# Kernel optimization log

Measured on AMD Instinct MI355X. Metric: run time of the kernel, lower is better.

## Reference

```python
import jax, jax.numpy as jnp
import numpy as np
import math

N_NODES = 50000
N_EDGES = 800000
IN_FEATS = 128
HID = 64
OUT = 2
D = 2  # num_layers


def calc_thetas(d):
    """Beta-distribution polynomial coefficients (ascending order), matching
    sympy.poly((x/2)**i * (1-x/2)**(d-i) / Beta(i+1, d+1-i)) with inverted coeffs."""
    thetas = []
    for i in range(d + 1):
        p1 = np.zeros(i + 1)
        p1[-1] = 0.5 ** i  # (x/2)^i, ascending coeffs
        p2 = np.array([math.comb(d - i, j) * (-0.5) ** j for j in range(d - i + 1)])  # (1-x/2)^(d-i)
        beta = math.factorial(i) * math.factorial(d - i) / math.factorial(d + 1)
        thetas.append((np.convolve(p1, p2) / beta).tolist())
    return thetas


def poly_branch(h, src, dst, thetas):
    """Run all PolyConv filters on activated features h; concat along feature dim."""
    n = h.shape[0]
    deg = jnp.zeros((n,), h.dtype).at[dst].add(jnp.ones((dst.shape[0],), h.dtype))
    dinv = jnp.clip(deg, 1.0, None) ** -0.5  # D^{-1/2} of in-degrees, clamped min 1
    dinv = dinv[:, None]
    outs = []
    for th in thetas:
        f = h
        acc = th[0] * h
        for k in range(1, len(th)):
            # feat <- feat - D^{-1/2} A D^{-1/2} feat  (copy_u / sum aggregation)
            agg = jax.ops.segment_sum((f * dinv)[src], dst, num_segments=n)
            f = f - agg * dinv
            acc = acc + th[k] * f
        outs.append(acc)
    return jnp.concatenate(outs, axis=-1)


def setup_inputs() -> dict:
    key = jax.random.key(0)
    ks = jax.random.split(key, 12)
    inp = {
        "x": jax.random.normal(ks[0], (N_NODES, IN_FEATS), jnp.float32),
        "sim_x": jax.random.normal(ks[1], (N_NODES, IN_FEATS), jnp.float32),
        "src": jax.random.randint(ks[2], (N_EDGES,), 0, N_NODES, jnp.int32),
        "dst": jax.random.randint(ks[3], (N_EDGES,), 0, N_NODES, jnp.int32),
        "sim_src": jax.random.randint(ks[4], (N_EDGES,), 0, N_NODES, jnp.int32),
        "sim_dst": jax.random.randint(ks[5], (N_EDGES,), 0, N_NODES, jnp.int32),
        "W1_o": jax.random.normal(ks[6], (IN_FEATS, HID), jnp.float32) / np.sqrt(IN_FEATS),
        "b1_o": jnp.zeros((HID,), jnp.float32),
        "W1_s": jax.random.normal(ks[7], (IN_FEATS, HID), jnp.float32) / np.sqrt(IN_FEATS),
        "b1_s": jnp.zeros((HID,), jnp.float32),
        "Wm1": jax.random.normal(ks[8], (HID * (D + 1) * 2, HID), jnp.float32) / np.sqrt(HID * (D + 1) * 2),
        "bm1": jnp.zeros((HID,), jnp.float32),
        "Wm2": jax.random.normal(ks[9], (HID, OUT), jnp.float32) / np.sqrt(HID),
        "bm2": jnp.zeros((OUT,), jnp.float32),
    }
    return inp


def reference(x, sim_x, src, dst, sim_src, sim_dst,
              W1_o, b1_o, W1_s, b1_s, Wm1, bm1, Wm2, bm2):
    thetas_o = calc_thetas(D)
    thetas_s = [[4.0] * (D + 1) for _ in range(D + 1)]  # conv_s uses constant theta=4

    h = jax.nn.relu(x @ W1_o + b1_o)
    h_final = poly_branch(h, src, dst, thetas_o)      # [N, HID*(D+1)]

    sh = jax.nn.relu(sim_x @ W1_s + b1_s)
    sim_h_final = poly_branch(sh, sim_src, sim_dst, thetas_s)

    h_all = jnp.concatenate([h_final, sim_h_final], axis=-1)  # [N, HID*(D+1)*2]
    logits = jax.nn.relu(h_all @ Wm1 + bm1) @ Wm2 + bm2
    return (h_all, logits)
```

## Files before the change

### kernel.cpp

```cpp
#include <hip/hip_runtime.h>
#include <hip/hip_fp16.h>


#define KB_BITS 10
#define KMAX 64
#define PCHUNK 4096
#define PVPT 16

__global__ __launch_bounds__(256) void bhist_kernel(
    const int* __restrict__ dst, const int* __restrict__ sim_dst,
    int* __restrict__ bhist, int E, int Es) {
    __shared__ int h[2 * KMAX];
    int tid = threadIdx.x;
    if (tid < 2 * KMAX) h[tid] = 0;
    __syncthreads();
    int total = E + Es;
    for (int e = blockIdx.x * 256 + tid; e < total; e += gridDim.x * 256) {
        if (e < E) atomicAdd(&h[dst[e] >> KB_BITS], 1);
        else       atomicAdd(&h[KMAX + (sim_dst[e - E] >> KB_BITS)], 1);
    }
    __syncthreads();
    if (tid < 2 * KMAX && h[tid]) atomicAdd(&bhist[tid], h[tid]);
}

__global__ __launch_bounds__(128) void bscan_kernel(
    const int* __restrict__ bhist, int* __restrict__ brow,
    int* __restrict__ gcur) {
    int g = threadIdx.x >> 6, lane = threadIdx.x & 63;
    int v = bhist[g * KMAX + lane];
    int inc = v;
    #pragma unroll
    for (int off = 1; off < 64; off <<= 1) {
        int u = __shfl_up(inc, off);
        if (lane >= off) inc += u;
    }
    int ex = inc - v;
    brow[g * (KMAX + 1) + lane] = ex;
    if (lane == 63) brow[g * (KMAX + 1) + KMAX] = inc;
    gcur[g * KMAX + lane] = ex;
}

__global__ __launch_bounds__(256) void partition_kernel(
    const int* __restrict__ src, const int* __restrict__ dst,
    const int* __restrict__ sim_src, const int* __restrict__ sim_dst,
    int* __restrict__ gcur, unsigned* __restrict__ staged,
    int E, int Es, int nbo) {
    int b = blockIdx.x;
    const int* S; const int* D; int Eg; int goff; unsigned* stg;
    if (b < nbo) { S = src; D = dst; Eg = E; goff = 0; stg = staged; }
    else { b -= nbo; S = sim_src; D = sim_dst; Eg = Es; goff = KMAX; stg = staged + E; }
    int e0 = b * PCHUNK;
    int cnt_blk = Eg - e0; if (cnt_blk > PCHUNK) cnt_blk = PCHUNK;
    __shared__ int hist[KMAX], basep[KMAX], cur[KMAX], gbase[KMAX];
    __shared__ unsigned srt[PCHUNK];
    int tid = threadIdx.x;
    if (tid < KMAX) hist[tid] = 0;
    __syncthreads();
    unsigned full[PVPT];
    #pragma unroll
    for (int i = 0; i < PVPT; ++i) {
        int idx = i * 256 + tid;
        if (idx < cnt_blk) {
            int e = e0 + idx;
            int d = D[e];
            unsigned bk = (unsigned)d >> KB_BITS;
            full[i] = (bk << 26) | ((unsigned)S[e] << KB_BITS) |
                      (unsigned)(d & ((1 << KB_BITS) - 1));
            atomicAdd(&hist[bk], 1);
        } else full[i] = 0xFFFFFFFFu;
    }
    __syncthreads();
    if (tid < 64) {
        int v = hist[tid];
        int inc = v;
        #pragma unroll
        for (int off = 1; off < 64; off <<= 1) {
            int u = __shfl_up(inc, off);
            if (tid >= off) inc += u;
        }
        int ex = inc - v;
        basep[tid] = ex;
        cur[tid] = ex;
        gbase[tid] = v ? atomicAdd(&gcur[goff + tid], v) : 0;
    }
    __syncthreads();
    #pragma unroll
    for (int i = 0; i < PVPT; ++i) {
        unsigned f = full[i];
        if (f != 0xFFFFFFFFu) {
            unsigned bk = f >> 26;
            int slot = atomicAdd(&cur[bk], 1);
            srt[slot] = f;
        }
    }
    __syncthreads();
    for (int slot = tid; slot < cnt_blk; slot += 256) {
        unsigned f = srt[slot];
        unsigned bk = f >> 26;
        int gpos = gbase[bk] + (slot - basep[bk]);
        stg[gpos] = f & 0x3FFFFFFu;
    }
}

__global__ __launch_bounds__(512) void place_kernel(
    const unsigned* __restrict__ staged, const int* __restrict__ brow,
    int* __restrict__ row_o, int* __restrict__ row_s,
    int* __restrict__ esrc_o, int* __restrict__ esrc_s,
    float* __restrict__ dinv, int N, int K, int E) {
    int b = blockIdx.x;
    const unsigned* stg; const int* br; int* row; int* esrc; float* dv;
    if (b < K) { stg = staged; br = brow; row = row_o; esrc = esrc_o; dv = dinv; }
    else { b -= K; stg = staged + E; br = brow + (KMAX + 1); row = row_s; esrc = esrc_s; dv = dinv + N; }
    int node0 = b << KB_BITS;
    int nn = N - node0; if (nn > (1 << KB_BITS)) nn = (1 << KB_BITS);
    int seg0 = br[b], seg1 = br[b + 1];
    __shared__ int ncnt[1 << KB_BITS];
    __shared__ int wsum[8];
    int tid = threadIdx.x;
    for (int i = tid; i < (1 << KB_BITS); i += 512) ncnt[i] = 0;
    __syncthreads();
    for (int j = seg0 + tid; j < seg1; j += 512)
        atomicAdd(&ncnt[stg[j] & ((1 << KB_BITS) - 1)], 1);
    __syncthreads();
    int i0 = tid * 2;
    int v0 = ncnt[i0], v1 = ncnt[i0 + 1];
    int s = v0 + v1;
    int inc = s;
    #pragma unroll
    for (int off = 1; off < 64; off <<= 1) {
        int u = __shfl_up(inc, off);
        if ((tid & 63) >= off) inc += u;
    }
    if ((tid & 63) == 63) wsum[tid >> 6] = inc;
    __syncthreads();
    int wo = 0;
    for (int w = 0; w < (tid >> 6); ++w) wo += wsum[w];
    int ex = seg0 + wo + inc - s;
    if (i0 < nn) {
        row[node0 + i0] = ex;
        dv[node0 + i0] = rsqrtf((float)(v0 > 1 ? v0 : 1));
    }
    if (i0 + 1 < nn) {
        row[node0 + i0 + 1] = ex + v0;
        dv[node0 + i0 + 1] = rsqrtf((float)(v1 > 1 ? v1 : 1));
    }
    if (b == K - 1 && tid == 0) row[N] = br[K];
    __syncthreads();
    ncnt[i0] = ex;
    ncnt[i0 + 1] = ex + v0;
    __syncthreads();
    for (int j = seg0 + tid; j < seg1; j += 512) {
        unsigned f = stg[j];
        int pos = atomicAdd(&ncnt[f & ((1 << KB_BITS) - 1)], 1);
        esrc[pos] = (int)(f >> KB_BITS);
    }
}

__global__ __launch_bounds__(256) void in_gemm_kernel(
    const float* __restrict__ x, const float* __restrict__ W,
    const float* __restrict__ b, float* __restrict__ out, int off,
    __half* __restrict__ h16, const float* __restrict__ dinvv, int n) {
    __shared__ float xs[64][132];
    __shared__ float Wf[128][68];
    int tid = threadIdx.x;
    int node0 = blockIdx.x * 64;
    const float4* wsrc = (const float4*)W;
    for (int i = tid; i < 2048; i += 256)
        *(float4*)&Wf[i >> 4][(i & 15) * 4] = wsrc[i];
    const float4* xsrc = (const float4*)x;
    for (int i = tid; i < 2048; i += 256) {
        int nl = i >> 5, c = i & 31;
        int node = node0 + nl;
        float4 v = make_float4(0.f, 0.f, 0.f, 0.f);
        if (node < n) v = xsrc[(long)node * 32 + c];
        *(float4*)&xs[nl][c * 4] = v;
    }
    __syncthreads();
    int tx = tid & 15, ty = tid >> 4;
    float acc[4][4] = {};
    #pragma unroll 2
    for (int k = 0; k < 128; k += 4) {
        float4 a[4], bb[4];
        #pragma unroll
        for (int i = 0; i < 4; ++i) a[i] = *(const float4*)&xs[ty * 4 + i][k];
        #pragma unroll
        for (int j = 0; j < 4; ++j) bb[j] = *(const float4*)&Wf[k + j][tx * 4];
        #pragma unroll
        for (int i = 0; i < 4; ++i) {
            acc[i][0] = fmaf(a[i].x, bb[0].x, acc[i][0]);
            acc[i][1] = fmaf(a[i].x, bb[0].y, acc[i][1]);
            acc[i][2] = fmaf(a[i].x, bb[0].z, acc[i][2]);
            acc[i][3] = fmaf(a[i].x, bb[0].w, acc[i][3]);
            acc[i][0] = fmaf(a[i].y, bb[1].x, acc[i][0]);
            acc[i][1] = fmaf(a[i].y, bb[1].y, acc[i][1]);
            acc[i][2] = fmaf(a[i].y, bb[1].z, acc[i][2]);
            acc[i][3] = fmaf(a[i].y, bb[1].w, acc[i][3]);
            acc[i][0] = fmaf(a[i].z, bb[2].x, acc[i][0]);
            acc[i][1] = fmaf(a[i].z, bb[2].y, acc[i][1]);
            acc[i][2] = fmaf(a[i].z, bb[2].z, acc[i][2]);
            acc[i][3] = fmaf(a[i].z, bb[2].w, acc[i][3]);
            acc[i][0] = fmaf(a[i].w, bb[3].x, acc[i][0]);
            acc[i][1] = fmaf(a[i].w, bb[3].y, acc[i][1]);
            acc[i][2] = fmaf(a[i].w, bb[3].z, acc[i][2]);
            acc[i][3] = fmaf(a[i].w, bb[3].w, acc[i][3]);
        }
    }
    float4 bias = *(const float4*)&b[tx * 4];
    #pragma unroll
    for (int i = 0; i < 4; ++i) {
        int node = node0 + ty * 4 + i;
        if (node >= n) break;
        float4 r;
        r.x = fmaxf(acc[i][0] + bias.x, 0.0f);
        r.y = fmaxf(acc[i][1] + bias.y, 0.0f);
        r.z = fmaxf(acc[i][2] + bias.z, 0.0f);
        r.w = fmaxf(acc[i][3] + bias.w, 0.0f);
        *(float4*)&out[(long)node * 384 + off + tx * 4] = r;
        if (h16) {
            float dvn = dinvv[node];
            __half hh[4];
            hh[0] = __float2half_rn(r.x * dvn);
            hh[1] = __float2half_rn(r.y * dvn);
            hh[2] = __float2half_rn(r.z * dvn);
            hh[3] = __float2half_rn(r.w * dvn);
            *(float2*)&h16[(long)node * 64 + tx * 4] = *(float2*)hh;
        }
    }
}

__global__ __launch_bounds__(256) void hop1_kernel(
    const int* __restrict__ row_o, const int* __restrict__ esrc_o, const float* __restrict__ dinv_o,
    const int* __restrict__ row_s, const int* __restrict__ esrc_s, const float* __restrict__ dinv_s,
    const __half* __restrict__ h16_o, const __half* __restrict__ h16_s,
    __half* __restrict__ g16_o, __half* __restrict__ g16_s,
    float* __restrict__ hall, int n, int nb) {
    int b = blockIdx.x;
    const int* row; const int* esrc; const float* dinv; const __half* h16; __half* g16; int base;
    if (b < nb) { row = row_o; esrc = esrc_o; dinv = dinv_o; h16 = h16_o; g16 = g16_o; base = 0; }
    else { b -= nb; row = row_s; esrc = esrc_s; dinv = dinv_s; h16 = h16_s; g16 = g16_s; base = 192; }
    int d = b * 4 + (threadIdx.x >> 6);
    if (d >= n) return;
    int lane = threadIdx.x & 63;
    int p = row[d], end = row[d + 1];
    long ob = (long)d * 384 + lane;
    float dd = dinv[d];
    float f0 = hall[ob + base];
    float a0 = 0.f, a1 = 0.f, a2 = 0.f, a3 = 0.f;
    for (; p + 8 <= end; p += 8) {
        int s0 = esrc[p], s1 = esrc[p + 1], s2 = esrc[p + 2], s3 = esrc[p + 3];
        int s4 = esrc[p + 4], s5 = esrc[p + 5], s6 = esrc[p + 6], s7 = esrc[p + 7];
        a0 += __half2float(h16[(long)s0 * 64 + lane]);
        a1 += __half2float(h16[(long)s1 * 64 + lane]);
        a2 += __half2float(h16[(long)s2 * 64 + lane]);
        a3 += __half2float(h16[(long)s3 * 64 + lane]);
        a0 += __half2float(h16[(long)s4 * 64 + lane]);
        a1 += __half2float(h16[(long)s5 * 64 + lane]);
        a2 += __half2float(h16[(long)s6 * 64 + lane]);
        a3 += __half2float(h16[(long)s7 * 64 + lane]);
    }
    for (; p < end; ++p) {
        int s = esrc[p];
        a0 += __half2float(h16[(long)s * 64 + lane]);
    }
    float acc = (a0 + a1) + (a2 + a3);
    float f1 = f0 - acc * dd;
    hall[ob + base + 64] = f1;
    g16[(long)d * 64 + lane] = __float2half_rn(f1 * dd);
}

__global__ __launch_bounds__(256) void hop2_kernel(
    const int* __restrict__ row_o, const int* __restrict__ esrc_o, const float* __restrict__ dinv_o,
    const int* __restrict__ row_s, const int* __restrict__ esrc_s, const float* __restrict__ dinv_s,
    const __half* __restrict__ g16_o, const __half* __restrict__ g16_s,
    float* __restrict__ hall, int n, int nb) {
    int b = blockIdx.x;
    bool ortho = b < nb;
    const int* row; const int* esrc; const float* dinv; const __half* g16; int base;
    if (ortho) { row = row_o; esrc = esrc_o; dinv = dinv_o; g16 = g16_o; base = 0; }
    else { b -= nb; row = row_s; esrc = esrc_s; dinv = dinv_s; g16 = g16_s; base = 192; }
    int d = b * 4 + (threadIdx.x >> 6);
    if (d >= n) return;
    int lane = threadIdx.x & 63;
    int p = row[d], end = row[d + 1];
    long ob = (long)d * 384 + lane;
    float dd = dinv[d];
    float f0 = hall[ob + base];
    float f1 = hall[ob + base + 64];
    float a0 = 0.f, a1 = 0.f, a2 = 0.f, a3 = 0.f;
    for (; p + 8 <= end; p += 8) {
        int s0 = esrc[p], s1 = esrc[p + 1], s2 = esrc[p + 2], s3 = esrc[p + 3];
        int s4 = esrc[p + 4], s5 = esrc[p + 5], s6 = esrc[p + 6], s7 = esrc[p + 7];
        a0 += __half2float(g16[(long)s0 * 64 + lane]);
        a1 += __half2float(g16[(long)s1 * 64 + lane]);
        a2 += __half2float(g16[(long)s2 * 64 + lane]);
        a3 += __half2float(g16[(long)s3 * 64 + lane]);
        a0 += __half2float(g16[(long)s4 * 64 + lane]);
        a1 += __half2float(g16[(long)s5 * 64 + lane]);
        a2 += __half2float(g16[(long)s6 * 64 + lane]);
        a3 += __half2float(g16[(long)s7 * 64 + lane]);
    }
    for (; p < end; ++p) {
        int s = esrc[p];
        a0 += __half2float(g16[(long)s * 64 + lane]);
    }
    float acc = (a0 + a1) + (a2 + a3);
    float f2 = f1 - acc * dd;
    if (ortho) {
        hall[ob]       = 3.0f * f0 - 3.0f * f1 + 0.75f * f2;
        hall[ob + 64]  = 3.0f * f1 - 1.5f * f2;
        hall[ob + 128] = 0.75f * f2;
    } else {
        float ss = 4.0f * (f0 + f1 + f2);
        hall[ob + 192] = ss; hall[ob + 256] = ss; hall[ob + 320] = ss;
    }
}

__global__ __launch_bounds__(256) void gather2_kernel(
    const int* __restrict__ row_o, const int* __restrict__ esrc_o, const float* __restrict__ dinv_o,
    const int* __restrict__ row_s, const int* __restrict__ esrc_s, const float* __restrict__ dinv_s,
    float* __restrict__ hall, int in_off_o, int in_off_s, int n, int nb) {
    int b = blockIdx.x;
    const int* row; const int* esrc; const float* dinv; int in_off;
    if (b < nb) { row = row_o; esrc = esrc_o; dinv = dinv_o; in_off = in_off_o; }
    else { b -= nb; row = row_s; esrc = esrc_s; dinv = dinv_s; in_off = in_off_s; }
    int d = b * 4 + (threadIdx.x >> 6);
    if (d >= n) return;
    int lane = threadIdx.x & 63;
    int p = row[d], end = row[d + 1];
    const float* fin = hall + in_off;
    float a0 = 0.f, a1 = 0.f, a2 = 0.f, a3 = 0.f;
    for (; p + 4 <= end; p += 4) {
        int s0 = esrc[p], s1 = esrc[p + 1], s2 = esrc[p + 2], s3 = esrc[p + 3];
        a0 = fmaf(fin[(long)s0 * 384 + lane], dinv[s0], a0);
        a1 = fmaf(fin[(long)s1 * 384 + lane], dinv[s1], a1);
        a2 = fmaf(fin[(long)s2 * 384 + lane], dinv[s2], a2);
        a3 = fmaf(fin[(long)s3 * 384 + lane], dinv[s3], a3);
    }
    for (; p < end; ++p) {
        int s = esrc[p];
        a0 = fmaf(fin[(long)s * 384 + lane], dinv[s], a0);
    }
    float acc = (a0 + a1) + (a2 + a3);
    long ob = (long)d * 384 + lane;
    hall[ob + in_off + 64] = fin[ob] - acc * dinv[d];
}

__global__ __launch_bounds__(256) void combine_kernel(float* __restrict__ h, int nf) {
    int i = blockIdx.x * 256 + threadIdx.x;
    if (i >= nf) return;
    long ob = (long)(i >> 6) * 384 + (i & 63);
    float f0v = h[ob], f1v = h[ob + 64], f2v = h[ob + 128];
    h[ob]       = 3.0f * f0v - 3.0f * f1v + 0.75f * f2v;
    h[ob + 64]  = 3.0f * f1v - 1.5f * f2v;
    h[ob + 128] = 0.75f * f2v;
    float ss = 4.0f * (h[ob + 192] + h[ob + 256] + h[ob + 320]);
    h[ob + 192] = ss; h[ob + 256] = ss; h[ob + 320] = ss;
}

__global__ __launch_bounds__(256) void mlp_kernel(
    const float* __restrict__ hall, const float* __restrict__ Wm1,
    const float* __restrict__ bm1, const float* __restrict__ Wm2,
    const float* __restrict__ bm2, float* __restrict__ logits, int n) {
    __shared__ float xs[64][132];
    __shared__ float Wf[128][68];
    int tid = threadIdx.x;
    int node0 = blockIdx.x * 64;
    int tx = tid & 15, ty = tid >> 4;
    float acc[4][4] = {};
    const float4* wsrc = (const float4*)Wm1;
    const float4* hsrc = (const float4*)hall;
    for (int c = 0; c < 3; ++c) {
        __syncthreads();
        for (int i = tid; i < 2048; i += 256)
            *(float4*)&Wf[i >> 4][(i & 15) * 4] = wsrc[c * 2048 + i];
        for (int i = tid; i < 2048; i += 256) {
            int nl = i >> 5, cc = i & 31;
            int node = node0 + nl;
            float4 v = make_float4(0.f, 0.f, 0.f, 0.f);
            if (node < n) v = hsrc[(long)node * 96 + c * 32 + cc];
            *(float4*)&xs[nl][cc * 4] = v;
        }
        __syncthreads();
        #pragma unroll 2
        for (int k = 0; k < 128; k += 4) {
            float4 a[4], bb[4];
            #pragma unroll
            for (int i = 0; i < 4; ++i) a[i] = *(const float4*)&xs[ty * 4 + i][k];
            #pragma unroll
            for (int j = 0; j < 4; ++j) bb[j] = *(const float4*)&Wf[k + j][tx * 4];
            #pragma unroll
            for (int i = 0; i < 4; ++i) {
                acc[i][0] = fmaf(a[i].x, bb[0].x, acc[i][0]);
                acc[i][1] = fmaf(a[i].x, bb[0].y, acc[i][1]);
                acc[i][2] = fmaf(a[i].x, bb[0].z, acc[i][2]);
                acc[i][3] = fmaf(a[i].x, bb[0].w, acc[i][3]);
                acc[i][0] = fmaf(a[i].y, bb[1].x, acc[i][0]);
                acc[i][1] = fmaf(a[i].y, bb[1].y, acc[i][1]);
                acc[i][2] = fmaf(a[i].y, bb[1].z, acc[i][2]);
                acc[i][3] = fmaf(a[i].y, bb[1].w, acc[i][3]);
                acc[i][0] = fmaf(a[i].z, bb[2].x, acc[i][0]);
                acc[i][1] = fmaf(a[i].z, bb[2].y, acc[i][1]);
                acc[i][2] = fmaf(a[i].z, bb[2].z, acc[i][2]);
                acc[i][3] = fmaf(a[i].z, bb[2].w, acc[i][3]);
                acc[i][0] = fmaf(a[i].w, bb[3].x, acc[i][0]);
                acc[i][1] = fmaf(a[i].w, bb[3].y, acc[i][1]);
                acc[i][2] = fmaf(a[i].w, bb[3].z, acc[i][2]);
                acc[i][3] = fmaf(a[i].w, bb[3].w, acc[i][3]);
            }
        }
    }
    __syncthreads();
    float4 bias = *(const float4*)&bm1[tx * 4];
    #pragma unroll
    for (int i = 0; i < 4; ++i) {
        xs[ty * 4 + i][tx * 4 + 0] = fmaxf(acc[i][0] + bias.x, 0.0f);
        xs[ty * 4 + i][tx * 4 + 1] = fmaxf(acc[i][1] + bias.y, 0.0f);
        xs[ty * 4 + i][tx * 4 + 2] = fmaxf(acc[i][2] + bias.z, 0.0f);
        xs[ty * 4 + i][tx * 4 + 3] = fmaxf(acc[i][3] + bias.w, 0.0f);
    }
    __syncthreads();
    if (tid < 128) {
        int nl = tid >> 1, o = tid & 1;
        int node = node0 + nl;
        if (node < n) {
            float p = bm2[o];
            #pragma unroll 8
            for (int k = 0; k < 64; ++k) p = fmaf(xs[nl][k], Wm2[k * 2 + o], p);
            logits[(long)node * 2 + o] = p;
        }
    }
}

extern "C" void kernel_launch(void* const* d_in, const int* in_sizes, int n_in,
                              void* d_out, int out_size, void* d_ws, size_t ws_size,
                              hipStream_t stream) {
    const float* x     = (const float*)d_in[0];
    const float* sim_x = (const float*)d_in[1];
    const int* src     = (const int*)d_in[2];
    const int* dst     = (const int*)d_in[3];
    const int* sim_src = (const int*)d_in[4];
    const int* sim_dst = (const int*)d_in[5];
    const float* W1_o = (const float*)d_in[6];
    const float* b1_o = (const float*)d_in[7];
    const float* W1_s = (const float*)d_in[8];
    const float* b1_s = (const float*)d_in[9];
    const float* Wm1  = (const float*)d_in[10];
    const float* bm1  = (const float*)d_in[11];
    const float* Wm2  = (const float*)d_in[12];
    const float* bm2  = (const float*)d_in[13];

    const int N  = in_sizes[0] / 128;
    const int E  = in_sizes[2];
    const int Es = in_sizes[4];
    const int NF = N * 64;
    const int K  = (N + (1 << KB_BITS) - 1) >> KB_BITS;

    float* hall = (float*)d_out;
    float* lgt  = hall + (long)N * 384;
    float* dinv = lgt;
    float* dinv_o = dinv;
    float* dinv_s = dinv + N;

    int* row_o  = (int*)d_ws;
    int* row_s  = row_o + (N + 1);
    int* esrc_o = row_s + (N + 1);
    int* esrc_s = esrc_o + E;
    int* bhist  = esrc_s + Es;
    int* brow   = bhist + 2 * KMAX;
    int* gcur   = brow + 2 * (KMAX + 1);
    __half* h16_o = (__half*)(gcur + 2 * KMAX);
    __half* h16_s = h16_o + (long)N * 64;
    __half* g16_o = h16_s + (long)N * 64;
    __half* g16_s = g16_o + (long)N * 64;
    size_t need_f16 = (size_t)((char*)(g16_s + (long)N * 64) - (char*)d_ws);
    bool f16path = ws_size >= need_f16;
    unsigned* staged = (unsigned*)h16_o;

    int nb4  = (N + 3) / 4;
    int nb64 = (N + 63) / 64;
    int nfb  = (NF + 255) / 256;
    int nbo  = (E + PCHUNK - 1) / PCHUNK;
    int nbs  = (Es + PCHUNK - 1) / PCHUNK;

    hipMemsetAsync(bhist, 0, (size_t)(2 * KMAX) * sizeof(int), stream);
    bhist_kernel<<<256, 256, 0, stream>>>(dst, sim_dst, bhist, E, Es);
    bscan_kernel<<<1, 128, 0, stream>>>(bhist, brow, gcur);
    partition_kernel<<<nbo + nbs, 256, 0, stream>>>(src, dst, sim_src, sim_dst,
                                                    gcur, staged, E, Es, nbo);
    place_kernel<<<2 * K, 512, 0, stream>>>(staged, brow, row_o, row_s,
                                            esrc_o, esrc_s, dinv, N, K, E);

    in_gemm_kernel<<<nb64, 256, 0, stream>>>(x, W1_o, b1_o, hall, 0,
                                             f16path ? h16_o : (__half*)nullptr, dinv_o, N);
    in_gemm_kernel<<<nb64, 256, 0, stream>>>(sim_x, W1_s, b1_s, hall, 192,
                                             f16path ? h16_s : (__half*)nullptr, dinv_s, N);

    if (f16path) {
        hop1_kernel<<<2 * nb4, 256, 0, stream>>>(row_o, esrc_o, dinv_o,
                                                 row_s, esrc_s, dinv_s,
                                                 h16_o, h16_s, g16_o, g16_s,
                                                 hall, N, nb4);
        hop2_kernel<<<2 * nb4, 256, 0, stream>>>(row_o, esrc_o, dinv_o,
                                                 row_s, esrc_s, dinv_s,
                                                 g16_o, g16_s, hall, N, nb4);
    } else {
        gather2_kernel<<<2 * nb4, 256, 0, stream>>>(row_o, esrc_o, dinv_o,
                                                    row_s, esrc_s, dinv_s,
                                                    hall, 0, 192, N, nb4);
        gather2_kernel<<<2 * nb4, 256, 0, stream>>>(row_o, esrc_o, dinv_o,
                                                    row_s, esrc_s, dinv_s,
                                                    hall, 64, 256, N, nb4);
        combine_kernel<<<nfb, 256, 0, stream>>>(hall, NF);
    }

    mlp_kernel<<<nb64, 256, 0, stream>>>(hall, Wm1, bm1, Wm2, bm2, lgt, N);
}
```

Baseline: 432.3 us.

## Drop fp32 intermediate traffic, recompute features from fp16, fold MLP weights

The input GEMM no longer writes fp32 features to the output on the fp16 path. The hop kernels rebuild f0 and f1 from the scaled fp16 buffers with sqrt(deg) and compute dinv from the CSR row extents. Block indices are interleaved so both graph branches run side by side. Since the sim branch writes three identical 4*(f0+f1+f2) columns, its three Wm1 slices are pre-summed so the MLP reads two K-chunks instead of three. This cuts global memory traffic and MLP FLOPs. The cost is that f0 and f1 now carry fp16 rounding, which may hurt accuracy.

```diff
diff --git a/kernel.cpp b/kernel.cpp
--- a/kernel.cpp
+++ b/kernel.cpp
@@ -154,6 +154,16 @@
         int pos = atomicAdd(&ncnt[f & ((1 << KB_BITS) - 1)], 1);
         esrc[pos] = (int)(f >> KB_BITS);
     }
+}
+
+__global__ __launch_bounds__(256) void fold_kernel(
+    const float* __restrict__ Wm1, float* __restrict__ w1f) {
+    int i = blockIdx.x * 256 + threadIdx.x;
+    if (i >= 256 * 64) return;
+    int k = i >> 6, j = i & 63;
+    float v = Wm1[k * 64 + j];
+    if (k >= 192) v += Wm1[(k + 64) * 64 + j] + Wm1[(k + 128) * 64 + j];
+    w1f[i] = v;
 }
 
 __global__ __launch_bounds__(256) void in_gemm_kernel(
@@ -215,7 +225,7 @@
         r.y = fmaxf(acc[i][1] + bias.y, 0.0f);
         r.z = fmaxf(acc[i][2] + bias.z, 0.0f);
         r.w = fmaxf(acc[i][3] + bias.w, 0.0f);
-        *(float4*)&out[(long)node * 384 + off + tx * 4] = r;
+        if (out) *(float4*)&out[(long)node * 384 + off + tx * 4] = r;
         if (h16) {
             float dvn = dinvv[node];
             __half hh[4];
@@ -229,22 +239,26 @@
 }
 
 __global__ __launch_bounds__(256) void hop1_kernel(
-    const int* __restrict__ row_o, const int* __restrict__ esrc_o, const float* __restrict__ dinv_o,
-    const int* __restrict__ row_s, const int* __restrict__ esrc_s, const float* __restrict__ dinv_s,
+    const int* __restrict__ row_o, const int* __restrict__ esrc_o,
+    const int* __restrict__ row_s, const int* __restrict__ esrc_s,
     const __half* __restrict__ h16_o, const __half* __restrict__ h16_s,
     __half* __restrict__ g16_o, __half* __restrict__ g16_s,
-    float* __restrict__ hall, int n, int nb) {
-    int b = blockIdx.x;
-    const int* row; const int* esrc; const float* dinv; const __half* h16; __half* g16; int base;
-    if (b < nb) { row = row_o; esrc = esrc_o; dinv = dinv_o; h16 = h16_o; g16 = g16_o; base = 0; }
-    else { b -= nb; row = row_s; esrc = esrc_s; dinv = dinv_s; h16 = h16_s; g16 = g16_s; base = 192; }
-    int d = b * 4 + (threadIdx.x >> 6);
+    int n, int nb4) {
+    int slot = blockIdx.x & 7;
+    int g = slot >> 2;
+    int bl = (blockIdx.x >> 3) * 4 + (slot & 3);
+    if (bl >= nb4) return;
+    const int* row; const int* esrc; const __half* h16; __half* g16;
+    if (g == 0) { row = row_o; esrc = esrc_o; h16 = h16_o; g16 = g16_o; }
+    else { row = row_s; esrc = esrc_s; h16 = h16_s; g16 = g16_s; }
+    int d = bl * 4 + (threadIdx.x >> 6);
     if (d >= n) return;
     int lane = threadIdx.x & 63;
     int p = row[d], end = row[d + 1];
-    long ob = (long)d * 384 + lane;
-    float dd = dinv[d];
-    float f0 = hall[ob + base];
+    int deg = end - p;
+    float degf = (float)(deg > 1 ? deg : 1);
+    float dd = rsqrtf(degf);
+    float h16v = __half2float(h16[(long)d * 64 + lane]);
     float a0 = 0.f, a1 = 0.f, a2 = 0.f, a3 = 0.f;
     for (; p + 8 <= end; p += 8) {
         int s0 = esrc[p], s1 = esrc[p + 1], s2 = esrc[p + 2], s3 = esrc[p + 3];
@@ -263,29 +277,32 @@
         a0 += __half2float(h16[(long)s * 64 + lane]);
     }
     float acc = (a0 + a1) + (a2 + a3);
-    float f1 = f0 - acc * dd;
-    hall[ob + base + 64] = f1;
-    g16[(long)d * 64 + lane] = __float2half_rn(f1 * dd);
+    g16[(long)d * 64 + lane] = __float2half_rn(h16v - acc * dd * dd);
 }
 
 __global__ __launch_bounds__(256) void hop2_kernel(
-    const int* __restrict__ row_o, const int* __restrict__ esrc_o, const float* __restrict__ dinv_o,
-    const int* __restrict__ row_s, const int* __restrict__ esrc_s, const float* __restrict__ dinv_s,
+    const int* __restrict__ row_o, const int* __restrict__ esrc_o,
+    const int* __restrict__ row_s, const int* __restrict__ esrc_s,
+    const __half* __restrict__ h16_o, const __half* __restrict__ h16_s,
     const __half* __restrict__ g16_o, const __half* __restrict__ g16_s,
-    float* __restrict__ hall, int n, int nb) {
-    int b = blockIdx.x;
-    bool ortho = b < nb;
-    const int* row; const int* esrc; const float* dinv; const __half* g16; int base;
-    if (ortho) { row = row_o; esrc = esrc_o; dinv = dinv_o; g16 = g16_o; base = 0; }
-    else { b -= nb; row = row_s; esrc = esrc_s; dinv = dinv_s; g16 = g16_s; base = 192; }
-    int d = b * 4 + (threadIdx.x >> 6);
+    float* __restrict__ hall, int n, int nb4) {
+    int slot = blockIdx.x & 7;
+    int g = slot >> 2;
+    int bl = (blockIdx.x >> 3) * 4 + (slot & 3);
+    if (bl >= nb4) return;
+    const int* row; const int* esrc; const __half* h16; const __half* g16; int base;
+    if (g == 0) { row = row_o; esrc = esrc_o; h16 = h16_o; g16 = g16_o; base = 0; }
+    else { row = row_s; esrc = esrc_s; h16 = h16_s; g16 = g16_s; base = 192; }
+    int d = bl * 4 + (threadIdx.x >> 6);
     if (d >= n) return;
     int lane = threadIdx.x & 63;
     int p = row[d], end = row[d + 1];
-    long ob = (long)d * 384 + lane;
-    float dd = dinv[d];
-    float f0 = hall[ob + base];
-    float f1 = hall[ob + base + 64];
+    int deg = end - p;
+    float degf = (float)(deg > 1 ? deg : 1);
+    float dd = rsqrtf(degf);
+    float sq = sqrtf(degf);
+    float f0 = __half2float(h16[(long)d * 64 + lane]) * sq;
+    float f1 = __half2float(g16[(long)d * 64 + lane]) * sq;
     float a0 = 0.f, a1 = 0.f, a2 = 0.f, a3 = 0.f;
     for (; p + 8 <= end; p += 8) {
         int s0 = esrc[p], s1 = esrc[p + 1], s2 = esrc[p + 2], s3 = esrc[p + 3];
@@ -305,7 +322,8 @@
     }
     float acc = (a0 + a1) + (a2 + a3);
     float f2 = f1 - acc * dd;
-    if (ortho) {
+    long ob = (long)d * 384 + lane;
+    if (g == 0) {
         hall[ob]       = 3.0f * f0 - 3.0f * f1 + 0.75f * f2;
         hall[ob + 64]  = 3.0f * f1 - 1.5f * f2;
         hall[ob + 128] = 0.75f * f2;
@@ -358,7 +376,7 @@
 }
 
 __global__ __launch_bounds__(256) void mlp_kernel(
-    const float* __restrict__ hall, const float* __restrict__ Wm1,
+    const float* __restrict__ hall, const float* __restrict__ w1f,
     const float* __restrict__ bm1, const float* __restrict__ Wm2,
     const float* __restrict__ bm2, float* __restrict__ logits, int n) {
     __shared__ float xs[64][132];
@@ -367,9 +385,9 @@
     int node0 = blockIdx.x * 64;
     int tx = tid & 15, ty = tid >> 4;
     float acc[4][4] = {};
-    const float4* wsrc = (const float4*)Wm1;
+    const float4* wsrc = (const float4*)w1f;
     const float4* hsrc = (const float4*)hall;
-    for (int c = 0; c < 3; ++c) {
+    for (int c = 0; c < 2; ++c) {
         __syncthreads();
         for (int i = tid; i < 2048; i += 256)
             *(float4*)&Wf[i >> 4][(i & 15) * 4] = wsrc[c * 2048 + i];
@@ -468,7 +486,8 @@
     int* bhist  = esrc_s + Es;
     int* brow   = bhist + 2 * KMAX;
     int* gcur   = brow + 2 * (KMAX + 1);
-    __half* h16_o = (__half*)(gcur + 2 * KMAX);
+    float* w1f  = (float*)(gcur + 2 * KMAX);
+    __half* h16_o = (__half*)(w1f + 256 * 64);
     __half* h16_s = h16_o + (long)N * 64;
     __half* g16_o = h16_s + (long)N * 64;
     __half* g16_s = g16_o + (long)N * 64;
@@ -477,12 +496,14 @@
     unsigned* staged = (unsigned*)h16_o;
 
     int nb4  = (N + 3) / 4;
+    int nbq  = (nb4 + 3) / 4;
     int nb64 = (N + 63) / 64;
     int nfb  = (NF + 255) / 256;
     int nbo  = (E + PCHUNK - 1) / PCHUNK;
     int nbs  = (Es + PCHUNK - 1) / PCHUNK;
 
     hipMemsetAsync(bhist, 0, (size_t)(2 * KMAX) * sizeof(int), stream);
+    fold_kernel<<<64, 256, 0, stream>>>(Wm1, w1f);
     bhist_kernel<<<256, 256, 0, stream>>>(dst, sim_dst, bhist, E, Es);
     bscan_kernel<<<1, 128, 0, stream>>>(bhist, brow, gcur);
     partition_kernel<<<nbo + nbs, 256, 0, stream>>>(src, dst, sim_src, sim_dst,
@@ -490,19 +511,19 @@
     place_kernel<<<2 * K, 512, 0, stream>>>(staged, brow, row_o, row_s,
                                             esrc_o, esrc_s, dinv, N, K, E);
 
-    in_gemm_kernel<<<nb64, 256, 0, stream>>>(x, W1_o, b1_o, hall, 0,
+    in_gemm_kernel<<<nb64, 256, 0, stream>>>(x, W1_o, b1_o,
+                                             f16path ? (float*)nullptr : hall, 0,
                                              f16path ? h16_o : (__half*)nullptr, dinv_o, N);
-    in_gemm_kernel<<<nb64, 256, 0, stream>>>(sim_x, W1_s, b1_s, hall, 192,
+    in_gemm_kernel<<<nb64, 256, 0, stream>>>(sim_x, W1_s, b1_s,
+                                             f16path ? (float*)nullptr : hall, 192,
                                              f16path ? h16_s : (__half*)nullptr, dinv_s, N);
 
     if (f16path) {
-        hop1_kernel<<<2 * nb4, 256, 0, stream>>>(row_o, esrc_o, dinv_o,
-                                                 row_s, esrc_s, dinv_s,
+        hop1_kernel<<<nbq * 8, 256, 0, stream>>>(row_o, esrc_o, row_s, esrc_s,
+                                                 h16_o, h16_s, g16_o, g16_s, N, nb4);
+        hop2_kernel<<<nbq * 8, 256, 0, stream>>>(row_o, esrc_o, row_s, esrc_s,
                                                  h16_o, h16_s, g16_o, g16_s,
                                                  hall, N, nb4);
-        hop2_kernel<<<2 * nb4, 256, 0, stream>>>(row_o, esrc_o, dinv_o,
-                                                 row_s, esrc_s, dinv_s,
-                                                 g16_o, g16_s, hall, N, nb4);
     } else {
         gather2_kernel<<<2 * nb4, 256, 0, stream>>>(row_o, esrc_o, dinv_o,
                                                     row_s, esrc_s, dinv_s,
@@ -513,5 +534,5 @@
         combine_kernel<<<nfb, 256, 0, stream>>>(hall, NF);
     }
 
-    mlp_kernel<<<nb64, 256, 0, stream>>>(hall, Wm1, bm1, Wm2, bm2, lgt, N);
-}
+    mlp_kernel<<<nb64, 256, 0, stream>>>(hall, w1f, bm1, Wm2, bm2, lgt, N);
+}
```

Measured after the change: 411.8 us. -4.7%, faster.
